# Kernel tuning notes

Measured on AMD Instinct MI355X. Metric: run time of the kernel, lower is better.

## Reference

```python
import jax, jax.numpy as jnp
import numpy as np

B_TAIL = 3.0  # 'bins' arg = tail bound of the spline interval [-B, B]


def _rqs_forward(u, w, h, d):
    """Rational-quadratic spline (Durkan et al.) with linear (identity) tails.
    u: (batch, dim); w,h: (dim, K); d: (dim, K-1). Returns x (batch, dim), logdet (batch,)."""
    dim, K = w.shape
    two_b = 2.0 * B_TAIL

    widths = jax.nn.softmax(w, axis=-1) * two_b                      # (dim, K)
    cum_w = jnp.concatenate(
        [jnp.full((dim, 1), -B_TAIL, u.dtype), -B_TAIL + jnp.cumsum(widths, axis=-1)],
        axis=-1)                                                     # (dim, K+1) knot x-positions
    cum_w = cum_w.at[:, -1].set(B_TAIL)

    heights = jax.nn.softmax(h, axis=-1) * two_b                     # (dim, K)
    cum_h = jnp.concatenate(
        [jnp.full((dim, 1), -B_TAIL, u.dtype), -B_TAIL + jnp.cumsum(heights, axis=-1)],
        axis=-1)                                                     # (dim, K+1) knot y-positions
    cum_h = cum_h.at[:, -1].set(B_TAIL)

    ones = jnp.ones((dim, 1), u.dtype)
    derivs = jnp.concatenate([ones, jax.nn.softplus(d), ones], axis=-1)  # (dim, K+1)

    inside = (u >= -B_TAIL) & (u <= B_TAIL)
    uc = jnp.clip(u, -B_TAIL, B_TAIL)

    # bin search: count interior knots <= uc  -> bin index in [0, K-1]
    idx = jnp.sum(uc[:, :, None] >= cum_w[None, :, 1:-1], axis=-1)   # (batch, dim) int32

    didx = jnp.arange(dim)[None, :]                                  # (1, dim)
    xk  = cum_w[didx, idx]
    wk  = widths[didx, idx]
    yk  = cum_h[didx, idx]
    hk  = heights[didx, idx]
    dk  = derivs[didx, idx]
    dk1 = derivs[didx, idx + 1]

    delta = hk / wk                                                  # bin slope
    theta = (uc - xk) / wk
    t1m = theta * (1.0 - theta)
    denom = delta + (dk + dk1 - 2.0 * delta) * t1m
    num = hk * (delta * theta * theta + dk * t1m)
    x_in = yk + num / denom

    ld_num = delta * delta * (dk1 * theta * theta + 2.0 * delta * t1m
                              + dk * (1.0 - theta) * (1.0 - theta))
    ld_in = jnp.log(ld_num) - 2.0 * jnp.log(denom)

    x = jnp.where(inside, x_in, u)          # identity linear tails
    ld = jnp.where(inside, ld_in, 0.0)
    return x, jnp.sum(ld, axis=-1)


def setup_inputs() -> dict:
    key = jax.random.key(0)
    ku, kw, kh, kd = jax.random.split(key, 4)
    batch, dim, K = 131072, 256, 5
    u = jax.random.normal(ku, (batch, dim), dtype=jnp.float32)
    w = jax.random.uniform(kw, (dim, K), dtype=jnp.float32, minval=-0.5, maxval=0.5)
    h = jax.random.uniform(kh, (dim, K), dtype=jnp.float32, minval=-0.5, maxval=0.5)
    d = jax.random.uniform(kd, (dim, K - 1), dtype=jnp.float32, minval=-0.5, maxval=0.5)
    return {"u": u, "w": w, "h": h, "d": d}


def reference(u, w, h, d):
    return _rqs_forward(u, w, h, d)
```

## Files before the change

kernel.cpp:

```cpp
#include <hip/hip_runtime.h>
#include <math.h>

#define BATCH 131072
#define DIM 256
#define NK 5
#define BT 3.0f
#define NBLK 1024
#define NTHR 512
#define ITERS 8

__global__ __launch_bounds__(NTHR, 8) void rqs_kernel(
    const float* __restrict__ u,
    const float* __restrict__ wp,
    const float* __restrict__ hp,
    const float* __restrict__ dp,
    float* __restrict__ x_out,
    float* __restrict__ ld_out)
{
    __shared__ float4 tabA[NK * DIM];
    __shared__ float4 tabB[NK * DIM];
    const int tid = threadIdx.x;

    if (tid < DIM) {
        const int dm = tid;
        float v[NK], wid[NK], xpos[NK], hei[NK], ypos[NK], dv[NK + 1];
        float mx, sum, scale, c;

        mx = -1e30f;
        #pragma unroll
        for (int k = 0; k < NK; k++) { v[k] = wp[dm * NK + k]; mx = fmaxf(mx, v[k]); }
        sum = 0.f;
        #pragma unroll
        for (int k = 0; k < NK; k++) { v[k] = expf(v[k] - mx); sum += v[k]; }
        scale = 6.0f / sum;
        c = -BT;
        #pragma unroll
        for (int k = 0; k < NK; k++) { wid[k] = v[k] * scale; xpos[k] = c; c += wid[k]; }

        mx = -1e30f;
        #pragma unroll
        for (int k = 0; k < NK; k++) { v[k] = hp[dm * NK + k]; mx = fmaxf(mx, v[k]); }
        sum = 0.f;
        #pragma unroll
        for (int k = 0; k < NK; k++) { v[k] = expf(v[k] - mx); sum += v[k]; }
        scale = 6.0f / sum;
        c = -BT;
        #pragma unroll
        for (int k = 0; k < NK; k++) { hei[k] = v[k] * scale; ypos[k] = c; c += hei[k]; }

        dv[0] = 1.0f; dv[NK] = 1.0f;
        #pragma unroll
        for (int k = 0; k < 4; k++) dv[1 + k] = log1pf(expf(dp[dm * 4 + k]));

        #pragma unroll
        for (int k = 0; k < NK; k++) {
            float iw  = 1.0f / wid[k];
            float dlt = hei[k] * iw;
            float dk  = dv[k], dk1 = dv[k + 1];
            tabA[k * DIM + dm] = make_float4(xpos[k], iw, dk + dk1 - 2.0f * dlt, dlt);
            tabB[k * DIM + dm] = make_float4(hei[k] * (dlt - dk), hei[k] * dk,
                                             ypos[k], 2.0f * (dlt - dk));
        }
    }
    __syncthreads();

    const int lane = tid & 63;
    const int wv   = tid >> 6;

    float kn[4][4];
    #pragma unroll
    for (int j = 0; j < 4; j++)
        #pragma unroll
        for (int i = 0; i < 4; i++)
            kn[j][i] = tabA[(i + 1) * DIM + lane + 64 * j].x;

    const int g = (blockIdx.x << 3) | wv;

    for (int it = 0; it < ITERS; it++) {
        const int r0 = (it << 14) | (g << 1);
        const float* up = u + (size_t)r0 * DIM + lane;

        float uin[2][4];
        #pragma unroll
        for (int rr = 0; rr < 2; rr++)
            #pragma unroll
            for (int j = 0; j < 4; j++)
                uin[rr][j] = up[rr * DIM + 64 * j];

        float ldacc0 = 0.f, ldacc1 = 0.f;

        #pragma unroll
        for (int rr = 0; rr < 2; rr++) {
            float uc[4];
            int   off[4];
            #pragma unroll
            for (int j = 0; j < 4; j++) {
                float uval = uin[rr][j];
                float c = fminf(fmaxf(uval, -BT), BT);
                int idx = (int)(c >= kn[j][0]) + (int)(c >= kn[j][1])
                        + (int)(c >= kn[j][2]) + (int)(c >= kn[j][3]);
                uc[j]  = c;
                off[j] = (idx << 8) + lane + (j << 6);
            }
            float4 A[4], Bv[4];
            #pragma unroll
            for (int j = 0; j < 4; j++) { A[j] = tabA[off[j]]; Bv[j] = tabB[off[j]]; }

            float xo[4];
            float lsum = 0.f;
            #pragma unroll
            for (int j = 0; j < 4; j++) {
                float xk = A[j].x,  iw = A[j].y,  s  = A[j].z,  dlt = A[j].w;
                float p  = Bv[j].x, q  = Bv[j].y, yk = Bv[j].z, rb  = Bv[j].w;

                float th    = (uc[j] - xk) * iw;
                float dk    = fmaf(-0.5f, rb, dlt);
                float r2    = dlt * dlt;
                float denom = fmaf(fmaf(-s, th, s), th, dlt);
                float invd  = __builtin_amdgcn_rcpf(denom);
                float num   = th * fmaf(p, th, q);
                float x_in  = fmaf(num, invd, yk);
                float ldq   = fmaf(fmaf(s, th, rb), th, dk);
                float ld    = __logf(ldq * r2 * invd * invd);

                xo[j] = (uc[j] == uin[rr][j]) ? x_in : uin[rr][j];
                lsum += ld;
            }
            if (rr == 0) ldacc0 = lsum; else ldacc1 = lsum;

            float* xp = x_out + (size_t)(r0 + rr) * DIM + lane;
            #pragma unroll
            for (int j = 0; j < 4; j++)
                __builtin_nontemporal_store(xo[j], xp + 64 * j);
        }

        #pragma unroll
        for (int sh = 32; sh > 0; sh >>= 1) {
            ldacc0 += __shfl_down(ldacc0, sh, 64);
            ldacc1 += __shfl_down(ldacc1, sh, 64);
        }
        if (lane == 0) {
            __builtin_nontemporal_store(ldacc0, ld_out + r0);
            __builtin_nontemporal_store(ldacc1, ld_out + r0 + 1);
        }
    }
}

extern "C" void kernel_launch(void* const* d_in, const int* in_sizes, int n_in,
                              void* d_out, int out_size, void* d_ws, size_t ws_size,
                              hipStream_t stream) {
    const float* u  = (const float*)d_in[0];
    const float* w  = (const float*)d_in[1];
    const float* h  = (const float*)d_in[2];
    const float* dd = (const float*)d_in[3];
    float* x  = (float*)d_out;
    float* ld = x + (size_t)BATCH * DIM;
    rqs_kernel<<<NBLK, NTHR, 0, stream>>>(u, w, h, dd, x, ld);
}
```

Measured before the change: 299.1 us.

## Vectorize u loads/x stores to float4 with permuted LDS table and prefetch

Each lane now handles four consecutive dims, loaded and stored as float4, so the kernel issues one 16-byte access per row per lane instead of four scalar accesses. The LDS coefficient tables are written in a permuted dim order so the per-column lookups still map to lane-contiguous LDS addresses. It also software-prefetches the next iteration's u rows into registers so their loads overlap the current computation. The cost is extra register pressure from the prefetched values.

```diff
diff --git a/kernel.cpp b/kernel.cpp
--- a/kernel.cpp
+++ b/kernel.cpp
@@ -8,6 +8,8 @@
 #define NBLK 1024
 #define NTHR 512
 #define ITERS 8
+
+typedef float f32x4 __attribute__((ext_vector_type(4)));
 
 __global__ __launch_bounds__(NTHR, 8) void rqs_kernel(
     const float* __restrict__ u,
@@ -52,13 +54,14 @@
         #pragma unroll
         for (int k = 0; k < 4; k++) dv[1 + k] = log1pf(expf(dp[dm * 4 + k]));
 
+        const int s_ = ((dm & 3) << 6) | (dm >> 2);
         #pragma unroll
         for (int k = 0; k < NK; k++) {
             float iw  = 1.0f / wid[k];
             float dlt = hei[k] * iw;
             float dk  = dv[k], dk1 = dv[k + 1];
-            tabA[k * DIM + dm] = make_float4(xpos[k], iw, dk + dk1 - 2.0f * dlt, dlt);
-            tabB[k * DIM + dm] = make_float4(hei[k] * (dlt - dk), hei[k] * dk,
+            tabA[k * DIM + s_] = make_float4(xpos[k], iw, dk + dk1 - 2.0f * dlt, dlt);
+            tabB[k * DIM + s_] = make_float4(hei[k] * (dlt - dk), hei[k] * dk,
                                              ypos[k], 2.0f * (dlt - dk));
         }
     }
@@ -69,51 +72,49 @@
 
     float kn[4][4];
     #pragma unroll
-    for (int j = 0; j < 4; j++)
+    for (int c = 0; c < 4; c++)
         #pragma unroll
         for (int i = 0; i < 4; i++)
-            kn[j][i] = tabA[(i + 1) * DIM + lane + 64 * j].x;
+            kn[c][i] = tabA[(i + 1) * DIM + (c << 6) + lane].x;
 
     const int g = (blockIdx.x << 3) | wv;
 
+    f32x4 uin[2];
+    {
+        const float* up = u + ((size_t)(g << 1)) * DIM + (lane << 2);
+        uin[0] = *(const f32x4*)up;
+        uin[1] = *(const f32x4*)(up + DIM);
+    }
+
     for (int it = 0; it < ITERS; it++) {
         const int r0 = (it << 14) | (g << 1);
-        const float* up = u + (size_t)r0 * DIM + lane;
 
-        float uin[2][4];
-        #pragma unroll
-        for (int rr = 0; rr < 2; rr++)
-            #pragma unroll
-            for (int j = 0; j < 4; j++)
-                uin[rr][j] = up[rr * DIM + 64 * j];
+        f32x4 unx[2];
+        if (it + 1 < ITERS) {
+            const float* up = u + ((size_t)(r0 + 16384)) * DIM + (lane << 2);
+            unx[0] = *(const f32x4*)up;
+            unx[1] = *(const f32x4*)(up + DIM);
+        }
 
         float ldacc0 = 0.f, ldacc1 = 0.f;
 
         #pragma unroll
         for (int rr = 0; rr < 2; rr++) {
-            float uc[4];
-            int   off[4];
-            #pragma unroll
-            for (int j = 0; j < 4; j++) {
-                float uval = uin[rr][j];
-                float c = fminf(fmaxf(uval, -BT), BT);
-                int idx = (int)(c >= kn[j][0]) + (int)(c >= kn[j][1])
-                        + (int)(c >= kn[j][2]) + (int)(c >= kn[j][3]);
-                uc[j]  = c;
-                off[j] = (idx << 8) + lane + (j << 6);
-            }
-            float4 A[4], Bv[4];
-            #pragma unroll
-            for (int j = 0; j < 4; j++) { A[j] = tabA[off[j]]; Bv[j] = tabB[off[j]]; }
-
-            float xo[4];
+            f32x4 xv;
             float lsum = 0.f;
             #pragma unroll
-            for (int j = 0; j < 4; j++) {
-                float xk = A[j].x,  iw = A[j].y,  s  = A[j].z,  dlt = A[j].w;
-                float p  = Bv[j].x, q  = Bv[j].y, yk = Bv[j].z, rb  = Bv[j].w;
+            for (int c = 0; c < 4; c++) {
+                float uval = uin[rr][c];
+                float uc = fminf(fmaxf(uval, -BT), BT);
+                int idx = (int)(uc >= kn[c][0]) + (int)(uc >= kn[c][1])
+                        + (int)(uc >= kn[c][2]) + (int)(uc >= kn[c][3]);
+                const int off = (idx << 8) + (c << 6) + lane;
+                float4 A  = tabA[off];
+                float4 Bv = tabB[off];
+                float xk = A.x,  iw = A.y,  s  = A.z,  dlt = A.w;
+                float p  = Bv.x, q  = Bv.y, yk = Bv.z, rb  = Bv.w;
 
-                float th    = (uc[j] - xk) * iw;
+                float th    = (uc - xk) * iw;
                 float dk    = fmaf(-0.5f, rb, dlt);
                 float r2    = dlt * dlt;
                 float denom = fmaf(fmaf(-s, th, s), th, dlt);
@@ -123,15 +124,13 @@
                 float ldq   = fmaf(fmaf(s, th, rb), th, dk);
                 float ld    = __logf(ldq * r2 * invd * invd);
 
-                xo[j] = (uc[j] == uin[rr][j]) ? x_in : uin[rr][j];
+                xv[c] = (uc == uval) ? x_in : uval;
                 lsum += ld;
             }
             if (rr == 0) ldacc0 = lsum; else ldacc1 = lsum;
 
-            float* xp = x_out + (size_t)(r0 + rr) * DIM + lane;
-            #pragma unroll
-            for (int j = 0; j < 4; j++)
-                __builtin_nontemporal_store(xo[j], xp + 64 * j);
+            __builtin_nontemporal_store(
+                xv, (f32x4*)(x_out + (size_t)(r0 + rr) * DIM + (lane << 2)));
         }
 
         #pragma unroll
@@ -142,6 +141,11 @@
         if (lane == 0) {
             __builtin_nontemporal_store(ldacc0, ld_out + r0);
             __builtin_nontemporal_store(ldacc1, ld_out + r0 + 1);
+        }
+
+        if (it + 1 < ITERS) {
+            uin[0] = unx[0];
+            uin[1] = unx[1];
         }
     }
 }
```

Measured after the change: 314.3 us. +5.1%, slower.
